# Kernel tuning notes

Measured on AMD Instinct MI355X. Metric: run time of the kernel, lower is better.

## Reference

```python
import jax, jax.numpy as jnp
from jax import lax
import numpy as np

B, N0 = 4, 4096
NIN, NH, NOUT = 16, 128, 2
DEPTH, K, RADIUS, KNN = 3, 64, 2.0, 3
EPS = 1e-5


def _bn(x, g, b):
    # eval-mode BatchNorm1d with running_mean=0, running_var=1
    return g * x / jnp.sqrt(1.0 + EPS) + b


def _mlp2(h, p):
    # Seq(Lin, ReLU, BN) x 2, as in MLP([d, d, out])
    w1, b1, g1, be1, w2, b2, g2, be2 = p
    h = _bn(jax.nn.relu(h @ w1 + b1), g1, be1)
    return _bn(jax.nn.relu(h @ w2 + b2), g2, be2)


def _fps(pts, m):
    # farthest point sampling, deterministic start at index 0
    n = pts.shape[0]
    def step(carry, _):
        dmin, last = carry
        d = jnp.sum((pts - pts[last]) ** 2, axis=-1)
        dmin = jnp.minimum(dmin, d)
        nxt = jnp.argmax(dmin).astype(jnp.int32)
        return (dmin, nxt), nxt
    _, rest = lax.scan(step, (jnp.full((n,), 1e30, pts.dtype), jnp.int32(0)), None, length=m - 1)
    return jnp.concatenate([jnp.zeros((1,), jnp.int32), rest])


def _sa(xx, pp, m, params):
    # SAModule with PointConv: fps -> radius(K nearest within r) -> gather-MLP-max
    idx = _fps(pp, m)
    q = pp[idx]                                              # [m,3] sampled centers
    d2 = jnp.sum((q[:, None, :] - pp[None, :, :]) ** 2, -1)  # [m,n]
    d2 = jnp.where(d2 <= RADIUS * RADIUS, d2, 1e30)
    neg, nbr = lax.top_k(-d2, K)                             # K nearest inside ball
    valid = neg > -1e29
    h = jnp.concatenate([xx[nbr], pp[nbr] - q[:, None, :]], axis=-1)  # [m,K,C+3]
    h = _mlp2(h, params)
    h = jnp.where(valid[..., None], h, -1e30)
    return jnp.max(h, axis=1), q                             # PointConv max aggr


def _fp(xx, pp, xs, ps, params):
    # FPModule: knn_interpolate (k=3, inverse squared-distance weights) + concat skip + MLP
    d2 = jnp.sum((ps[:, None, :] - pp[None, :, :]) ** 2, -1)  # [n_fine, n_coarse]
    neg, idx = lax.top_k(-d2, KNN)
    w = 1.0 / jnp.maximum(-neg, 1e-16)
    y = jnp.sum(w[..., None] * xx[idx], axis=1) / jnp.sum(w, axis=1, keepdims=True)
    return _mlp2(jnp.concatenate([y, xs], axis=-1), params)


def _forward(x, pos, lin_in_w, lin_in_b,
             sa_w1, sa_b1, sa_g1, sa_be1, sa_w2, sa_b2, sa_g2, sa_be2,
             fp_w1, fp_b1, fp_g1, fp_be1, fp_w2, fp_b2, fp_g2, fp_be2,
             lo_w1, lo_b1, lo_g1, lo_be1, lo_w2, lo_b2, lo_g2, lo_be2):
    xb = jax.nn.relu(x.reshape(B, N0, NIN) @ lin_in_w + lin_in_b)  # lin_in + ReLU
    posb = pos.reshape(B, N0, 3)
    sa = [(xb, posb)]
    n = N0
    for i in range(DEPTH):
        m = n // 2  # ratio = 0.5
        p = (sa_w1[i], sa_b1[i], sa_g1[i], sa_be1[i], sa_w2[i], sa_b2[i], sa_g2[i], sa_be2[i])
        h, q = jax.vmap(lambda a, b: _sa(a, b, m, p))(sa[i][0], sa[i][1])
        sa.append((h, q))
        n = m
    xf, posf = sa[DEPTH]
    for step in range(DEPTH):
        mi = DEPTH - 1 - step
        xs, ps = sa[DEPTH - 1 - step]
        p = (fp_w1[mi], fp_b1[mi], fp_g1[mi], fp_be1[mi], fp_w2[mi], fp_b2[mi], fp_g2[mi], fp_be2[mi])
        xf = jax.vmap(lambda a, b, c, d: _fp(a, b, c, d, p))(xf, posf, xs, ps)
        posf = ps
    out = _mlp2(xf, (lo_w1, lo_b1, lo_g1, lo_be1, lo_w2, lo_b2, lo_g2, lo_be2))
    return out.reshape(B * N0, NOUT)


def setup_inputs() -> dict:
    key = jax.random.key(0)
    ki = iter(jax.random.split(key, 24))
    def nrm(shape, s=0.1):
        return jax.random.normal(next(ki), shape, jnp.float32) * s
    D = NH + 3   # PointConv MLP in-dim
    F = 2 * NH   # FP MLP in-dim (nIn + nSkip)
    return {
        "x": jax.random.normal(next(ki), (B * N0, NIN), jnp.float32),
        "pos": jax.random.uniform(next(ki), (B * N0, 3), jnp.float32) * 16.0,
        "batch": jnp.repeat(jnp.arange(B, dtype=jnp.int32), N0),
        "lin_in_w": nrm((NIN, NH)), "lin_in_b": nrm((NH,)),
        "sa_w1": nrm((DEPTH, D, D)), "sa_b1": nrm((DEPTH, D)),
        "sa_g1": jnp.ones((DEPTH, D)), "sa_be1": jnp.zeros((DEPTH, D)),
        "sa_w2": nrm((DEPTH, D, NH)), "sa_b2": nrm((DEPTH, NH)),
        "sa_g2": jnp.ones((DEPTH, NH)), "sa_be2": jnp.zeros((DEPTH, NH)),
        "fp_w1": nrm((DEPTH, F, F)), "fp_b1": nrm((DEPTH, F)),
        "fp_g1": jnp.ones((DEPTH, F)), "fp_be1": jnp.zeros((DEPTH, F)),
        "fp_w2": nrm((DEPTH, F, NH)), "fp_b2": nrm((DEPTH, NH)),
        "fp_g2": jnp.ones((DEPTH, NH)), "fp_be2": jnp.zeros((DEPTH, NH)),
        "lo_w1": nrm((NH, NH)), "lo_b1": nrm((NH,)),
        "lo_g1": jnp.ones((NH,)), "lo_be1": jnp.zeros((NH,)),
        "lo_w2": nrm((NH, NOUT)), "lo_b2": nrm((NOUT,)),
        "lo_g2": jnp.ones((NOUT,)), "lo_be2": jnp.zeros((NOUT,)),
    }


def reference(x, pos, batch, lin_in_w, lin_in_b,
              sa_w1, sa_b1, sa_g1, sa_be1, sa_w2, sa_b2, sa_g2, sa_be2,
              fp_w1, fp_b1, fp_g1, fp_be1, fp_w2, fp_b2, fp_g2, fp_be2,
              lo_w1, lo_b1, lo_g1, lo_be1, lo_w2, lo_b2, lo_g2, lo_be2):
    return _forward(x, pos, lin_in_w, lin_in_b,
                    sa_w1, sa_b1, sa_g1, sa_be1, sa_w2, sa_b2, sa_g2, sa_be2,
                    fp_w1, fp_b1, fp_g1, fp_be1, fp_w2, fp_b2, fp_g2, fp_be2,
                    lo_w1, lo_b1, lo_g1, lo_be1, lo_w2, lo_b2, lo_g2, lo_be2)
```

## Files before the change

kernel.cpp:

```cpp
#include <hip/hip_runtime.h>
#include <cstddef>


#define EPSF 1e-5f

__device__ __forceinline__ float d2_rn(float dx, float dy, float dz) {
    return __fadd_rn(__fadd_rn(__fmul_rn(dx, dx), __fmul_rn(dy, dy)), __fmul_rn(dz, dz));
}

template <int CTRL, int RMASK>
__device__ __forceinline__ float dpp_max_f32(float v) {
    int o = __builtin_amdgcn_update_dpp(__float_as_int(v), __float_as_int(v),
                                        CTRL, RMASK, 0xf, false);
    return fmaxf(v, __int_as_float(o));
}

template <int N, int NT>
__device__ void fps_role(const float* __restrict__ pts, float* __restrict__ q,
                         const int m, const int b, char* smem) {
    constexpr int PPT = N / NT;
    constexpr int NW = NT / 64;
    float* s_px = (float*)smem;
    float* s_py = s_px + N;
    float* s_pz = s_py + N;
    int*   s_qi = (int*)(s_pz + N);
    float2* s_slot = (float2*)(s_qi + N / 2);
    const int t = threadIdx.x;
    const int wave = t >> 6, lane = t & 63;
    const int base = t * PPT;
    const float* P = pts + (size_t)b * N * 3;
    asm volatile("s_setprio 3");
    float rx[PPT], ry[PPT], rz[PPT], dmin[PPT];
#pragma unroll
    for (int j = 0; j < PPT; ++j) {
        int i = base + j;
        float x = P[i * 3], y = P[i * 3 + 1], z = P[i * 3 + 2];
        rx[j] = x; ry[j] = y; rz[j] = z; dmin[j] = 1e30f;
        s_px[i] = x; s_py[i] = y; s_pz[i] = z;
    }
    float lx = P[0], ly = P[1], lz = P[2];
    if (t == 0) s_qi[0] = 0;

    for (int step = 1; step < m; ++step) {
        float bv = -1.0f; int bj = 0;
#pragma unroll
        for (int j = 0; j < PPT; ++j) {
            float d = d2_rn(rx[j] - lx, ry[j] - ly, rz[j] - lz);
            float dm = fminf(dmin[j], d);
            dmin[j] = dm;
            if (dm > bv) { bv = dm; bj = j; }
        }
        const int bidx = base + bj;

        float v = bv;
        v = dpp_max_f32<0x111, 0xf>(v);
        v = dpp_max_f32<0x112, 0xf>(v);
        v = dpp_max_f32<0x114, 0xf>(v);
        v = dpp_max_f32<0x118, 0xf>(v);
        v = dpp_max_f32<0x142, 0xa>(v);
        v = dpp_max_f32<0x143, 0xc>(v);
        const float mv = __int_as_float(__builtin_amdgcn_readlane(__float_as_int(v), 63));
        unsigned long long mb = __ballot(bv == mv);
        const int wl = __ffsll((long long)mb) - 1;
        const int wbi = __builtin_amdgcn_readlane(bidx, wl);

        const int p = step & 1;
        if (lane == 0) s_slot[p * NW + wave] = make_float2(mv, __int_as_float(wbi));
        __syncthreads();

        float2 sl = s_slot[p * NW + (lane & (NW - 1))];
        float gvt = sl.x;
        gvt = dpp_max_f32<0x111, 0xf>(gvt);
        gvt = dpp_max_f32<0x112, 0xf>(gvt);
        if (NW == 8) gvt = dpp_max_f32<0x114, 0xf>(gvt);
        const float gm = __int_as_float(
            __builtin_amdgcn_readlane(__float_as_int(gvt), NW - 1));
        unsigned long long gb = __ballot((lane < NW) && (sl.x == gm));
        const int gl = __ffsll((long long)gb) - 1;
        const int gi = __builtin_amdgcn_readlane(__float_as_int(sl.y), gl);

        lx = s_px[gi]; ly = s_py[gi]; lz = s_pz[gi];
        if (t == 0) s_qi[step] = gi;
    }
    __syncthreads();
    for (int e = t; e < m; e += NT) {
        int gi = s_qi[e];
        size_t o = ((size_t)b * m + e) * 3;
        q[o] = s_px[gi]; q[o + 1] = s_py[gi]; q[o + 2] = s_pz[gi];
    }
}

__device__ void lin_role(const float* __restrict__ x, const float* __restrict__ w,
                         const float* __restrict__ bias, float* __restrict__ xb,
                         const int blk) {
    const int t = threadIdx.x;
    const int row = blk * 2 + (t >> 7);
    const int col = t & 127;
    float acc = bias[col];
#pragma unroll
    for (int k = 0; k < 16; ++k) acc = fmaf(x[row * 16 + k], w[k * 128 + col], acc);
    xb[row * 128 + col] = fmaxf(acc, 0.0f);
}

template <int CHUNK, int WACT>
__device__ void nbr_role(const float* __restrict__ pts, const float* __restrict__ q,
                         int2* __restrict__ pairs, unsigned* __restrict__ counter,
                         const int n, const int m, const int blk, char* smem) {
    const int w = threadIdx.x >> 6, lane = threadIdx.x & 63;
    if (w >= WACT) return;
    float* D = (float*)smem + w * CHUNK * 64;
    const int c = blk * WACT + w;
    const int b = c / m;
    const float* P = pts + (size_t)b * n * 3;
    const float qx = q[(size_t)c * 3 + 0];
    const float qy = q[(size_t)c * 3 + 1];
    const float qz = q[(size_t)c * 3 + 2];
    for (int s = 0; s < CHUNK; ++s) {
        int i = s * 64 + lane;
        float d2 = d2_rn(P[i * 3] - qx, P[i * 3 + 1] - qy, P[i * 3 + 2] - qz);
        D[i] = (d2 <= 4.0f) ? d2 : 1e30f;
    }
    int my_g = -1;
    int cnt = 0;
    for (int round = 0; round < 64; ++round) {
        float bv = 3e38f;
        int bi = 0x7fffffff;
        for (int s = 0; s < CHUNK; ++s) {
            int i = s * 64 + lane;
            float v = D[i];
            if (v < bv) { bv = v; bi = i; }
        }
#pragma unroll
        for (int off = 32; off >= 1; off >>= 1) {
            float ov = __shfl_xor(bv, off, 64);
            int   oi = __shfl_xor(bi, off, 64);
            if (ov < bv || (ov == bv && oi < bi)) { bv = ov; bi = oi; }
        }
        if (bv > 1e29f) break;
        if (round == lane) my_g = bi;
        if (lane == (bi & 63)) D[bi] = 3e38f;
        ++cnt;
    }
    unsigned base = 0;
    if (lane == 0) base = atomicAdd(counter, (unsigned)cnt);
    base = (unsigned)__shfl((int)base, 0, 64);
    if (lane < cnt) pairs[base + lane] = make_int2(c, my_g);
}

typedef float Row132[132];
__device__ void sa_body(const float* __restrict__ xx, const float* __restrict__ pts,
    const float* __restrict__ q, const int2* __restrict__ pairs,
    const unsigned* __restrict__ vcount,
    const float* __restrict__ w1, const float* __restrict__ b1,
    const float* __restrict__ g1, const float* __restrict__ be1,
    const float* __restrict__ w2, const float* __restrict__ b2,
    const float* __restrict__ g2, const float* __restrict__ be2,
    float* __restrict__ hout, const int lm, const int ln, const int blk, char* smem) {
    Row132* shA = (Row132*)smem;
    Row132* shW = (Row132*)(smem + 33792);
    int* sh_c = (int*)(smem + 50688);
    int* sh_g = sh_c + 64;
    const int t = threadIdx.x;
    const int V = (int)*vcount;
    const int r0 = blk * 64;
    if (r0 >= V) return;
    if (t < 64) {
        int r = r0 + t;
        if (r < V) { int2 p = pairs[r]; sh_c[t] = p.x; sh_g[t] = p.y; }
        else { sh_c[t] = -1; sh_g[t] = 0; }
    }
    __syncthreads();

    for (int e = t; e < 64 * 33; e += 256) {
        int row = e / 33, cid = e - row * 33;
        int c = sh_c[row];
        float4 v = make_float4(0.f, 0.f, 0.f, 0.f);
        if (c >= 0) {
            int g = sh_g[row];
            int b = c >> lm;
            size_t pt = ((size_t)(b << ln) + g);
            if (cid < 32) {
                v = *(const float4*)(xx + (pt << 7) + cid * 4);
            } else {
                const float* P = pts + pt * 3;
                const float* Q = q + (size_t)c * 3;
                v.x = P[0] - Q[0]; v.y = P[1] - Q[1]; v.z = P[2] - Q[2]; v.w = 0.f;
            }
        }
        *(float4*)&shA[row][cid * 4] = v;
    }
    __syncthreads();

    const float invs = 1.0f / sqrtf(1.0f + EPSF);
    const int tr = t >> 4, tc = t & 15;
    const int xrow = t >> 2, xcol = t & 3;
    float acc[32];
#pragma unroll
    for (int i = 0; i < 32; ++i) acc[i] = 0.0f;
    float accx = 0.0f;

    for (int k0 = 0; k0 < 132; k0 += 32) {
        const int kc = (132 - k0 < 32) ? (132 - k0) : 32;
        for (int e = t; e < kc * 132; e += 256) {
            int kk = e / 132, j = e - kk * 132;
            int k = k0 + kk;
            shW[kk][j] = (k < 131 && j < 131) ? w1[k * 131 + j] : 0.0f;
        }
        __syncthreads();
        for (int kk = 0; kk < kc; kk += 4) {
            const int k = k0 + kk;
            const float4 A0 = *(const float4*)&shA[tr     ][k];
            const float4 A1 = *(const float4*)&shA[tr + 16][k];
            const float4 A2 = *(const float4*)&shA[tr + 32][k];
            const float4 A3 = *(const float4*)&shA[tr + 48][k];
            const float4 AX = *(const float4*)&shA[xrow][k];
            const float a0v[4] = {A0.x, A0.y, A0.z, A0.w};
            const float a1v[4] = {A1.x, A1.y, A1.z, A1.w};
            const float a2v[4] = {A2.x, A2.y, A2.z, A2.w};
            const float a3v[4] = {A3.x, A3.y, A3.z, A3.w};
            const float axv[4] = {AX.x, AX.y, AX.z, AX.w};
#pragma unroll
            for (int u = 0; u < 4; ++u) {
                const float4 w0 = *(const float4*)&shW[kk + u][8 * tc];
                const float4 w1v = *(const float4*)&shW[kk + u][8 * tc + 4];
                const float wa[8] = {w0.x, w0.y, w0.z, w0.w, w1v.x, w1v.y, w1v.z, w1v.w};
#pragma unroll
                for (int j = 0; j < 8; ++j) {
                    acc[0 * 8 + j] = fmaf(a0v[u], wa[j], acc[0 * 8 + j]);
                    acc[1 * 8 + j] = fmaf(a1v[u], wa[j], acc[1 * 8 + j]);
                    acc[2 * 8 + j] = fmaf(a2v[u], wa[j], acc[2 * 8 + j]);
                    acc[3 * 8 + j] = fmaf(a3v[u], wa[j], acc[3 * 8 + j]);
                }
                accx = fmaf(axv[u], shW[kk + u][128 + xcol], accx);
            }
        }
        __syncthreads();
    }
#pragma unroll
    for (int i = 0; i < 4; ++i)
#pragma unroll
        for (int j = 0; j < 8; ++j) {
            int col = 8 * tc + j;
            float z = fmaxf(acc[i * 8 + j] + b1[col], 0.0f);
            shA[tr + 16 * i][col] = g1[col] * z * invs + be1[col];
        }
    if (xcol < 3) {
        int col = 128 + xcol;
        float z = fmaxf(accx + b1[col], 0.0f);
        shA[xrow][col] = g1[col] * z * invs + be1[col];
    } else {
        shA[xrow][131] = 0.0f;
    }

#pragma unroll
    for (int i = 0; i < 32; ++i) acc[i] = 0.0f;
    for (int k0 = 0; k0 < 132; k0 += 32) {
        const int kc = (132 - k0 < 32) ? (132 - k0) : 32;
        for (int e = t; e < kc * 132; e += 256) {
            int kk = e / 132, j = e - kk * 132;
            int k = k0 + kk;
            shW[kk][j] = (k < 131 && j < 128) ? w2[k * 128 + j] : 0.0f;
        }
        __syncthreads();
        for (int kk = 0; kk < kc; kk += 4) {
            const int k = k0 + kk;
            const float4 A0 = *(const float4*)&shA[tr     ][k];
            const float4 A1 = *(const float4*)&shA[tr + 16][k];
            const float4 A2 = *(const float4*)&shA[tr + 32][k];
            const float4 A3 = *(const float4*)&shA[tr + 48][k];
            const float a0v[4] = {A0.x, A0.y, A0.z, A0.w};
            const float a1v[4] = {A1.x, A1.y, A1.z, A1.w};
            const float a2v[4] = {A2.x, A2.y, A2.z, A2.w};
            const float a3v[4] = {A3.x, A3.y, A3.z, A3.w};
#pragma unroll
            for (int u = 0; u < 4; ++u) {
                const float4 w0 = *(const float4*)&shW[kk + u][8 * tc];
                const float4 w1v = *(const float4*)&shW[kk + u][8 * tc + 4];
                const float wa[8] = {w0.x, w0.y, w0.z, w0.w, w1v.x, w1v.y, w1v.z, w1v.w};
#pragma unroll
                for (int j = 0; j < 8; ++j) {
                    acc[0 * 8 + j] = fmaf(a0v[u], wa[j], acc[0 * 8 + j]);
                    acc[1 * 8 + j] = fmaf(a1v[u], wa[j], acc[1 * 8 + j]);
                    acc[2 * 8 + j] = fmaf(a2v[u], wa[j], acc[2 * 8 + j]);
                    acc[3 * 8 + j] = fmaf(a3v[u], wa[j], acc[3 * 8 + j]);
                }
            }
        }
        __syncthreads();
    }
#pragma unroll
    for (int i = 0; i < 4; ++i)
#pragma unroll
        for (int j = 0; j < 8; ++j) {
            int col = 8 * tc + j;
            float z = fmaxf(acc[i * 8 + j] + b2[col], 0.0f);
            shA[tr + 16 * i][col] = g2[col] * z * invs + be2[col];
        }
    __syncthreads();

    if (t < 128) {
        const int col = t;
        float run = -1.0f;
        int cur = sh_c[0];
        for (int row = 0; row < 64; ++row) {
            int c = sh_c[row];
            if (c != cur) {
                if (cur >= 0)
                    atomicMax((unsigned*)&hout[((size_t)cur << 7) + col], __float_as_uint(run));
                run = -1.0f; cur = c;
            }
            run = fmaxf(run, shA[row][col]);
        }
        if (cur >= 0)
            atomicMax((unsigned*)&hout[((size_t)cur << 7) + col], __float_as_uint(run));
    }
}

__device__ void knn_role(const float* __restrict__ pf, const float* __restrict__ pc,
                         int* __restrict__ kidx, float* __restrict__ kw,
                         const int nf, const int nc, const int blk) {
    const int tg = blk * 256 + threadIdx.x;
    const int b = tg / nf;
    const float* F = pf + (size_t)tg * 3;
    const float fx = F[0], fy = F[1], fz = F[2];
    const float* C = pc + (size_t)b * nc * 3;
    float b0 = 1e30f, b1 = 1e30f, b2 = 1e30f;
    int i0 = 0, i1 = 0, i2 = 0;
    for (int j = 0; j < nc; ++j) {
        float d2 = d2_rn(C[j * 3] - fx, C[j * 3 + 1] - fy, C[j * 3 + 2] - fz);
        if (d2 < b0)      { b2 = b1; i2 = i1; b1 = b0; i1 = i0; b0 = d2; i0 = j; }
        else if (d2 < b1) { b2 = b1; i2 = i1; b1 = d2; i1 = j; }
        else if (d2 < b2) { b2 = d2; i2 = j; }
    }
    float w0 = 1.0f / fmaxf(b0, 1e-16f);
    float w1 = 1.0f / fmaxf(b1, 1e-16f);
    float w2 = 1.0f / fmaxf(b2, 1e-16f);
    float inv = 1.0f / (w0 + w1 + w2);
    size_t o = (size_t)tg * 3;
    kidx[o] = i0; kidx[o + 1] = i1; kidx[o + 2] = i2;
    kw[o] = w0 * inv; kw[o + 1] = w1 * inv; kw[o + 2] = w2 * inv;
}

__global__ __launch_bounds__(256) void stage_a_kernel(
    const float* __restrict__ pos, float* __restrict__ q1,
    const float* __restrict__ x, const float* __restrict__ lin_w,
    const float* __restrict__ lin_b, float* __restrict__ xb,
    float* __restrict__ hbuf, unsigned* __restrict__ ctrs) {
    __shared__ __align__(16) char smem[57408];
    const int blk = blockIdx.x;
    if (blk < 4) {
        fps_role<4096, 256>(pos, q1, 2048, blk, smem);
    } else if (blk < 4 + 8192) {
        lin_role(x, lin_w, lin_b, xb, blk - 4);
    } else {
        const int i = blk - 8196;
        *(float4*)(hbuf + (size_t)i * 1024 + threadIdx.x * 4) =
            make_float4(0.f, 0.f, 0.f, 0.f);
        if (i == 0 && threadIdx.x < 3) ctrs[threadIdx.x * 16] = 0u;
    }
}

__global__ __launch_bounds__(256) void stage_b_kernel(
    const float* __restrict__ q1, float* __restrict__ q2,
    const float* __restrict__ pos, int2* __restrict__ pairs1,
    unsigned* __restrict__ ctr0,
    int* __restrict__ kidx2, float* __restrict__ kw2) {
    __shared__ __align__(16) char smem[32768];
    const int blk = blockIdx.x;
    if (blk < 4) fps_role<2048, 256>(q1, q2, 1024, blk, smem);
    else if (blk < 4 + 4096)
        nbr_role<64, 2>(pos, q1, pairs1, ctr0, 4096, 2048, blk - 4, smem);
    else
        knn_role(pos, q1, kidx2, kw2, 4096, 2048, blk - 4100);
}

__global__ __launch_bounds__(256) void stage_c_kernel(
    const float* __restrict__ q2, float* __restrict__ q3,
    const float* __restrict__ q1, int2* __restrict__ pairs2,
    unsigned* __restrict__ ctr1,
    const float* __restrict__ xb, const float* __restrict__ pos,
    const int2* __restrict__ pairs1, const unsigned* __restrict__ ctr0,
    const float* __restrict__ w1, const float* __restrict__ b1,
    const float* __restrict__ g1, const float* __restrict__ be1,
    const float* __restrict__ w2, const float* __restrict__ b2,
    const float* __restrict__ g2, const float* __restrict__ be2,
    float* __restrict__ h1, int* __restrict__ kidx1, float* __restrict__ kw1) {
    __shared__ __align__(16) char smem[51200];
    const int blk = blockIdx.x;
    if (blk < 4) fps_role<1024, 256>(q2, q3, 512, blk, smem);
    else if (blk < 4 + 1024)
        nbr_role<32, 4>(q1, q2, pairs2, ctr1, 2048, 1024, blk - 4, smem);
    else if (blk < 4 + 1024 + 8192)
        sa_body(xb, pos, q1, pairs1, ctr0, w1, b1, g1, be1, w2, b2, g2, be2,
                h1, 11, 12, blk - 1028, smem);
    else
        knn_role(q1, q2, kidx1, kw1, 2048, 1024, blk - 9220);
}

__global__ __launch_bounds__(256) void stage_d_kernel(
    const float* __restrict__ q2, const float* __restrict__ q3,
    int2* __restrict__ pairs3, unsigned* __restrict__ ctr2,
    const float* __restrict__ h1, const float* __restrict__ q1,
    const int2* __restrict__ pairs2, const unsigned* __restrict__ ctr1,
    const float* __restrict__ w1, const float* __restrict__ b1,
    const float* __restrict__ g1, const float* __restrict__ be1,
    const float* __restrict__ w2, const float* __restrict__ b2,
    const float* __restrict__ g2, const float* __restrict__ be2,
    float* __restrict__ h2, int* __restrict__ kidx0, float* __restrict__ kw0) {
    __shared__ __align__(16) char smem[51200];
    const int blk = blockIdx.x;
    if (blk < 512) nbr_role<16, 4>(q2, q3, pairs3, ctr2, 1024, 512, blk, smem);
    else if (blk < 512 + 16) knn_role(q2, q3, kidx0, kw0, 1024, 512, blk - 512);
    else
        sa_body(h1, q1, q2, pairs2, ctr1, w1, b1, g1, be1, w2, b2, g2, be2,
                h2, 10, 11, blk - 528, smem);
}

__global__ __launch_bounds__(256) void sa_fused_kernel(
    const float* xx, const float* pts, const float* q, const int2* pairs,
    const unsigned* vcount,
    const float* w1, const float* b1, const float* g1, const float* be1,
    const float* w2, const float* b2, const float* g2, const float* be2,
    float* hout, int lm, int ln) {
    __shared__ __align__(16) char smem[51200];
    sa_body(xx, pts, q, pairs, vcount, w1, b1, g1, be1, w2, b2, g2, be2,
            hout, lm, ln, blockIdx.x, smem);
}

__global__ __launch_bounds__(256) void fp_fused_kernel(
    const float* __restrict__ xc, const float* __restrict__ xs,
    const int* __restrict__ kidx, const float* __restrict__ kw,
    const float* __restrict__ w1, const float* __restrict__ b1,
    const float* __restrict__ g1, const float* __restrict__ be1,
    const float* __restrict__ w2, const float* __restrict__ b2,
    const float* __restrict__ g2, const float* __restrict__ be2,
    float* __restrict__ out, int lnf) {
    __shared__ __align__(16) float shA[32][260];
    __shared__ __align__(16) float shW[16][256];
    const int t = threadIdx.x;
    const int r0 = blockIdx.x * 32;
    const float invs = 1.0f / sqrtf(1.0f + EPSF);

    for (int e = t; e < 32 * 64; e += 256) {
        int r = e >> 6, cid = e & 63;
        int fr = r0 + r;
        float4 v;
        if (cid < 32) {
            int b = fr >> lnf;
            size_t o = (size_t)fr * 3;
            int i0 = kidx[o], i1 = kidx[o + 1], i2 = kidx[o + 2];
            float u0 = kw[o], u1 = kw[o + 1], u2 = kw[o + 2];
            const float* X = xc + (((size_t)b << lnf) >> 1) * 128;
            const float4 A0 = *(const float4*)(X + (size_t)i0 * 128 + cid * 4);
            const float4 A1 = *(const float4*)(X + (size_t)i1 * 128 + cid * 4);
            const float4 A2 = *(const float4*)(X + (size_t)i2 * 128 + cid * 4);
            v.x = u0 * A0.x + u1 * A1.x + u2 * A2.x;
            v.y = u0 * A0.y + u1 * A1.y + u2 * A2.y;
            v.z = u0 * A0.z + u1 * A1.z + u2 * A2.z;
            v.w = u0 * A0.w + u1 * A1.w + u2 * A2.w;
        } else {
            v = *(const float4*)(xs + (size_t)fr * 128 + (cid - 32) * 4);
        }
        *(float4*)&shA[r][cid * 4] = v;
    }
    __syncthreads();

    const int tr = t >> 5, tc = t & 31;
    float acc[32];
#pragma unroll
    for (int i = 0; i < 32; ++i) acc[i] = 0.0f;
    for (int k0 = 0; k0 < 256; k0 += 16) {
        for (int e = t; e < 16 * 64; e += 256) {
            int kk = e >> 6, cid = e & 63;
            *(float4*)&shW[kk][cid * 4] =
                *(const float4*)(w1 + (size_t)(k0 + kk) * 256 + cid * 4);
        }
        __syncthreads();
        for (int kk = 0; kk < 16; kk += 4) {
            const int k = k0 + kk;
            const float4 A0 = *(const float4*)&shA[tr     ][k];
            const float4 A1 = *(const float4*)&shA[tr +  8][k];
            const float4 A2 = *(const float4*)&shA[tr + 16][k];
            const float4 A3 = *(const float4*)&shA[tr + 24][k];
            const float a0v[4] = {A0.x, A0.y, A0.z, A0.w};
            const float a1v[4] = {A1.x, A1.y, A1.z, A1.w};
            const float a2v[4] = {A2.x, A2.y, A2.z, A2.w};
            const float a3v[4] = {A3.x, A3.y, A3.z, A3.w};
#pragma unroll
            for (int u = 0; u < 4; ++u) {
                const float4 w0v = *(const float4*)&shW[kk + u][8 * tc];
                const float4 w1v = *(const float4*)&shW[kk + u][8 * tc + 4];
                const float wa[8] = {w0v.x, w0v.y, w0v.z, w0v.w, w1v.x, w1v.y, w1v.z, w1v.w};
#pragma unroll
                for (int j = 0; j < 8; ++j) {
                    acc[0 * 8 + j] = fmaf(a0v[u], wa[j], acc[0 * 8 + j]);
                    acc[1 * 8 + j] = fmaf(a1v[u], wa[j], acc[1 * 8 + j]);
                    acc[2 * 8 + j] = fmaf(a2v[u], wa[j], acc[2 * 8 + j]);
                    acc[3 * 8 + j] = fmaf(a3v[u], wa[j], acc[3 * 8 + j]);
                }
            }
        }
        __syncthreads();
    }
#pragma unroll
    for (int i = 0; i < 4; ++i)
#pragma unroll
        for (int j = 0; j < 8; ++j) {
            int col = 8 * tc + j;
            float z = fmaxf(acc[i * 8 + j] + b1[col], 0.0f);
            shA[tr + 8 * i][col] = g1[col] * z * invs + be1[col];
        }
    __syncthreads();

    const int tr2 = t >> 4, tc2 = t & 15;
    float acc2[16];
#pragma unroll
    for (int i = 0; i < 16; ++i) acc2[i] = 0.0f;
    for (int k0 = 0; k0 < 256; k0 += 16) {
        for (int e = t; e < 16 * 32; e += 256) {
            int kk = e >> 5, cid = e & 31;
            *(float4*)&shW[kk][cid * 4] =
                *(const float4*)(w2 + (size_t)(k0 + kk) * 128 + cid * 4);
        }
        __syncthreads();
        for (int kk = 0; kk < 16; kk += 4) {
            const int k = k0 + kk;
            const float4 A0 = *(const float4*)&shA[tr2     ][k];
            const float4 A1 = *(const float4*)&shA[tr2 + 16][k];
            const float a0v[4] = {A0.x, A0.y, A0.z, A0.w};
            const float a1v[4] = {A1.x, A1.y, A1.z, A1.w};
#pragma unroll
            for (int u = 0; u < 4; ++u) {
                const float4 w0v = *(const float4*)&shW[kk + u][8 * tc2];
                const float4 w1v = *(const float4*)&shW[kk + u][8 * tc2 + 4];
                const float wa[8] = {w0v.x, w0v.y, w0v.z, w0v.w, w1v.x, w1v.y, w1v.z, w1v.w};
#pragma unroll
                for (int j = 0; j < 8; ++j) {
                    acc2[0 * 8 + j] = fmaf(a0v[u], wa[j], acc2[0 * 8 + j]);
                    acc2[1 * 8 + j] = fmaf(a1v[u], wa[j], acc2[1 * 8 + j]);
                }
            }
        }
        __syncthreads();
    }
#pragma unroll
    for (int i = 0; i < 2; ++i)
#pragma unroll
        for (int j = 0; j < 8; ++j) {
            int col = 8 * tc2 + j;
            int fr = r0 + tr2 + 16 * i;
            float z = fmaxf(acc2[i * 8 + j] + b2[col], 0.0f);
            out[(size_t)fr * 128 + col] = g2[col] * z * invs + be2[col];
        }
}

__global__ __launch_bounds__(256) void lo_fused_kernel(
    const float* __restrict__ in,
    const float* __restrict__ w1, const float* __restrict__ b1,
    const float* __restrict__ g1, const float* __restrict__ be1,
    const float* __restrict__ w2, const float* __restrict__ b2,
    const float* __restrict__ g2, const float* __restrict__ be2,
    float* __restrict__ out) {
    __shared__ __align__(16) float shA[32][132];
    __shared__ __align__(16) float shW[16][128];
    const int t = threadIdx.x;
    const int r0 = blockIdx.x * 32;
    const float invs = 1.0f / sqrtf(1.0f + EPSF);

    for (int e = t; e < 32 * 32; e += 256) {
        int r = e >> 5, cid = e & 31;
        *(float4*)&shA[r][cid * 4] =
            *(const float4*)(in + (size_t)(r0 + r) * 128 + cid * 4);
    }
    __syncthreads();

    const int tr = t >> 4, tc = t & 15;
    float acc[16];
#pragma unroll
    for (int i = 0; i < 16; ++i) acc[i] = 0.0f;
    for (int k0 = 0; k0 < 128; k0 += 16) {
        for (int e = t; e < 16 * 32; e += 256) {
            int kk = e >> 5, cid = e & 31;
            *(float4*)&shW[kk][cid * 4] =
                *(const float4*)(w1 + (size_t)(k0 + kk) * 128 + cid * 4);
        }
        __syncthreads();
        for (int kk = 0; kk < 16; ++kk) {
            const int k = k0 + kk;
            float a0 = shA[2 * tr + 0][k], a1 = shA[2 * tr + 1][k];
            const float4 w0v = *(const float4*)&shW[kk][8 * tc];
            const float4 w1v = *(const float4*)&shW[kk][8 * tc + 4];
            const float wa[8] = {w0v.x, w0v.y, w0v.z, w0v.w, w1v.x, w1v.y, w1v.z, w1v.w};
#pragma unroll
            for (int j = 0; j < 8; ++j) {
                acc[0 * 8 + j] = fmaf(a0, wa[j], acc[0 * 8 + j]);
                acc[1 * 8 + j] = fmaf(a1, wa[j], acc[1 * 8 + j]);
            }
        }
        __syncthreads();
    }
#pragma unroll
    for (int i = 0; i < 2; ++i)
#pragma unroll
        for (int j = 0; j < 8; ++j) {
            int col = 8 * tc + j;
            float z = fmaxf(acc[i * 8 + j] + b1[col], 0.0f);
            shA[2 * tr + i][col] = g1[col] * z * invs + be1[col];
        }
    __syncthreads();

    if (t < 64) {
        const int row = t >> 1, col = t & 1;
        float a = b2[col];
        for (int k = 0; k < 128; ++k)
            a = fmaf(shA[row][k], w2[k * 2 + col], a);
        a = fmaxf(a, 0.0f);
        out[(size_t)(r0 + row) * 2 + col] = g2[col] * a * invs + be2[col];
    }
}

extern "C" void kernel_launch(void* const* d_in, const int* in_sizes, int n_in,
                              void* d_out, int out_size, void* d_ws, size_t ws_size,
                              hipStream_t stream) {
    const float* x      = (const float*)d_in[0];
    const float* pos    = (const float*)d_in[1];
    const float* lin_w  = (const float*)d_in[3];
    const float* lin_b  = (const float*)d_in[4];
    const float* sa_w1  = (const float*)d_in[5];
    const float* sa_b1  = (const float*)d_in[6];
    const float* sa_g1  = (const float*)d_in[7];
    const float* sa_be1 = (const float*)d_in[8];
    const float* sa_w2  = (const float*)d_in[9];
    const float* sa_b2  = (const float*)d_in[10];
    const float* sa_g2  = (const float*)d_in[11];
    const float* sa_be2 = (const float*)d_in[12];
    const float* fp_w1  = (const float*)d_in[13];
    const float* fp_b1  = (const float*)d_in[14];
    const float* fp_g1  = (const float*)d_in[15];
    const float* fp_be1 = (const float*)d_in[16];
    const float* fp_w2  = (const float*)d_in[17];
    const float* fp_b2  = (const float*)d_in[18];
    const float* fp_g2  = (const float*)d_in[19];
    const float* fp_be2 = (const float*)d_in[20];
    const float* lo_w1  = (const float*)d_in[21];
    const float* lo_b1  = (const float*)d_in[22];
    const float* lo_g1  = (const float*)d_in[23];
    const float* lo_be1 = (const float*)d_in[24];
    const float* lo_w2  = (const float*)d_in[25];
    const float* lo_b2  = (const float*)d_in[26];
    const float* lo_g2  = (const float*)d_in[27];
    const float* lo_be2 = (const float*)d_in[28];

    float* ws = (float*)d_ws;
    size_t off = 0;
    auto alloc = [&](size_t n) { float* p = ws + off; off += n; return p; };
    float* xb    = alloc(4 * 4096 * 128);
    float* q1    = alloc(4 * 2048 * 3);
    float* q2    = alloc(4 * 1024 * 3);
    float* q3    = alloc(4 * 512 * 3);
    float* h1    = alloc(4 * 2048 * 128);
    float* h2    = alloc(4 * 1024 * 128);
    float* h3    = alloc(4 * 512 * 128);
    int2* pairs1 = (int2*)alloc(4 * 2048 * 64 * 2);
    int2* pairs2 = (int2*)alloc(4 * 1024 * 64 * 2);
    int2* pairs3 = (int2*)alloc(4 * 512 * 64 * 2);
    unsigned* ctrs = (unsigned*)alloc(64);
    int* kidx0   = (int*)alloc(4 * 1024 * 3);
    float* kw0   = alloc(4 * 1024 * 3);
    int* kidx1   = (int*)alloc(4 * 2048 * 3);
    float* kw1   = alloc(4 * 2048 * 3);
    int* kidx2   = (int*)alloc(4 * 4096 * 3);
    float* kw2   = alloc(4 * 4096 * 3);
    float* xfA   = alloc(4 * 4096 * 128);
    float* xfB   = alloc(4 * 4096 * 128);
    if (ws_size < off * sizeof(float)) return;

    stage_a_kernel<<<4 + 8192 + 1792, 256, 0, stream>>>(
        pos, q1, x, lin_w, lin_b, xb, h1, ctrs);

    stage_b_kernel<<<4 + 4096 + 64, 256, 0, stream>>>(
        q1, q2, pos, pairs1, ctrs + 0, kidx2, kw2);

    stage_c_kernel<<<4 + 1024 + 8192 + 32, 256, 0, stream>>>(
        q2, q3, q1, pairs2, ctrs + 16,
        xb, pos, pairs1, ctrs + 0,
        sa_w1, sa_b1, sa_g1, sa_be1, sa_w2, sa_b2, sa_g2, sa_be2, h1,
        kidx1, kw1);

    stage_d_kernel<<<512 + 16 + 4096, 256, 0, stream>>>(
        q2, q3, pairs3, ctrs + 32,
        h1, q1, pairs2, ctrs + 16,
        sa_w1 + 131 * 131, sa_b1 + 131, sa_g1 + 131, sa_be1 + 131,
        sa_w2 + 131 * 128, sa_b2 + 128, sa_g2 + 128, sa_be2 + 128, h2,
        kidx0, kw0);

    sa_fused_kernel<<<2048, 256, 0, stream>>>(h2, q2, q3, pairs3, ctrs + 32,
        sa_w1 + 2 * 131 * 131, sa_b1 + 2 * 131, sa_g1 + 2 * 131, sa_be1 + 2 * 131,
        sa_w2 + 2 * 131 * 128, sa_b2 + 2 * 128, sa_g2 + 2 * 128, sa_be2 + 2 * 128,
        h3, 9, 10);

    fp_fused_kernel<<<4 * 1024 / 32, 256, 0, stream>>>(h3, h2, kidx0, kw0,
        fp_w1 + 2 * 256 * 256, fp_b1 + 2 * 256, fp_g1 + 2 * 256, fp_be1 + 2 * 256,
        fp_w2 + 2 * 256 * 128, fp_b2 + 2 * 128, fp_g2 + 2 * 128, fp_be2 + 2 * 128,
        xfA, 10);

    fp_fused_kernel<<<4 * 2048 / 32, 256, 0, stream>>>(xfA, h1, kidx1, kw1,
        fp_w1 + 256 * 256, fp_b1 + 256, fp_g1 + 256, fp_be1 + 256,
        fp_w2 + 256 * 128, fp_b2 + 128, fp_g2 + 128, fp_be2 + 128,
        xfB, 11);

    fp_fused_kernel<<<4 * 4096 / 32, 256, 0, stream>>>(xfB, xb, kidx2, kw2,
        fp_w1, fp_b1, fp_g1, fp_be1, fp_w2, fp_b2, fp_g2, fp_be2,
        xfA, 12);

    lo_fused_kernel<<<16384 / 32, 256, 0, stream>>>(xfA,
        lo_w1, lo_b1, lo_g1, lo_be1, lo_w2, lo_b2, lo_g2, lo_be2,
        (float*)d_out);
}
```

Baseline: 3.346 ms.

## Replace FPS per-step barrier with tagged LDS spin-wait and packed-key reduction

The farthest-point-sampling loop no longer calls __syncthreads every step. Each wave publishes its best value together with a step-tagged, index-packed key into double-buffered volatile LDS slots, and readers spin until every slot carries the current tag. The cross-wave argmax becomes a 64-bit packed-key max over xor shuffles, and point coordinates move to a float4 LDS layout so one load fetches them. This targets the barrier latency on the serial FPS critical path, at the cost of busy-wait polling and a larger static LDS footprint, which could lower occupancy for the other roles sharing these kernels.

```diff
diff --git a/kernel.cpp b/kernel.cpp
--- a/kernel.cpp
+++ b/kernel.cpp
@@ -20,11 +20,10 @@
                          const int m, const int b, char* smem) {
     constexpr int PPT = N / NT;
     constexpr int NW = NT / 64;
-    float* s_px = (float*)smem;
-    float* s_py = s_px + N;
-    float* s_pz = s_py + N;
-    int*   s_qi = (int*)(s_pz + N);
-    float2* s_slot = (float2*)(s_qi + N / 2);
+    float4* s_p4 = (float4*)smem;
+    int*    s_qi = (int*)(s_p4 + N);
+    volatile unsigned* s_lo = (volatile unsigned*)(s_qi + N / 2);
+    volatile unsigned* s_hi = s_lo + 2 * NW;
     const int t = threadIdx.x;
     const int wave = t >> 6, lane = t & 63;
     const int base = t * PPT;
@@ -36,10 +35,12 @@
         int i = base + j;
         float x = P[i * 3], y = P[i * 3 + 1], z = P[i * 3 + 2];
         rx[j] = x; ry[j] = y; rz[j] = z; dmin[j] = 1e30f;
-        s_px[i] = x; s_py[i] = y; s_pz[i] = z;
-    }
+        s_p4[i] = make_float4(x, y, z, 0.0f);
+    }
+    if (t == 0) s_qi[0] = 0;
+    if (t < 2 * NW) { s_lo[t] = 0u; s_hi[t] = 0u; }
+    __syncthreads();
     float lx = P[0], ly = P[1], lz = P[2];
-    if (t == 0) s_qi[0] = 0;
 
     for (int step = 1; step < m; ++step) {
         float bv = -1.0f; int bj = 0;
@@ -64,29 +65,39 @@
         const int wl = __ffsll((long long)mb) - 1;
         const int wbi = __builtin_amdgcn_readlane(bidx, wl);
 
-        const int p = step & 1;
-        if (lane == 0) s_slot[p * NW + wave] = make_float2(mv, __int_as_float(wbi));
-        __syncthreads();
-
-        float2 sl = s_slot[p * NW + (lane & (NW - 1))];
-        float gvt = sl.x;
-        gvt = dpp_max_f32<0x111, 0xf>(gvt);
-        gvt = dpp_max_f32<0x112, 0xf>(gvt);
-        if (NW == 8) gvt = dpp_max_f32<0x114, 0xf>(gvt);
-        const float gm = __int_as_float(
-            __builtin_amdgcn_readlane(__float_as_int(gvt), NW - 1));
-        unsigned long long gb = __ballot((lane < NW) && (sl.x == gm));
-        const int gl = __ffsll((long long)gb) - 1;
-        const int gi = __builtin_amdgcn_readlane(__float_as_int(sl.y), gl);
-
-        lx = s_px[gi]; ly = s_py[gi]; lz = s_pz[gi];
+        const unsigned tag = (unsigned)(step & 0xff);
+        const int p = (step & 1) * NW;
+        if (lane == 0) {
+            s_hi[p + wave] = (unsigned)__float_as_int(mv);
+            s_lo[p + wave] = ((unsigned)(4095 - wbi) << 14) | ((unsigned)wave << 8) | tag;
+        }
+        const int sl = p + (lane & (NW - 1));
+        unsigned lo, hi;
+        do {
+            lo = s_lo[sl];
+            hi = s_hi[sl];
+        } while (__any((lo & 0xffu) != tag));
+
+        unsigned long long kv = ((unsigned long long)hi << 32) | lo;
+#pragma unroll
+        for (int off = 1; off < NW; off <<= 1) {
+            unsigned olo = (unsigned)__shfl_xor((int)(unsigned)(kv & 0xffffffffu), off, 64);
+            unsigned ohi = (unsigned)__shfl_xor((int)(unsigned)(kv >> 32), off, 64);
+            unsigned long long ov = ((unsigned long long)ohi << 32) | olo;
+            if (ov > kv) kv = ov;
+        }
+        const int gi = 4095 - (int)((kv >> 14) & 0xfffu);
+
+        const float4 pw = s_p4[gi];
+        lx = pw.x; ly = pw.y; lz = pw.z;
         if (t == 0) s_qi[step] = gi;
     }
     __syncthreads();
     for (int e = t; e < m; e += NT) {
         int gi = s_qi[e];
         size_t o = ((size_t)b * m + e) * 3;
-        q[o] = s_px[gi]; q[o + 1] = s_py[gi]; q[o + 2] = s_pz[gi];
+        float4 pw = s_p4[gi];
+        q[o] = pw.x; q[o + 1] = pw.y; q[o + 2] = pw.z;
     }
 }
 
@@ -346,7 +357,7 @@
     const float* __restrict__ x, const float* __restrict__ lin_w,
     const float* __restrict__ lin_b, float* __restrict__ xb,
     float* __restrict__ hbuf, unsigned* __restrict__ ctrs) {
-    __shared__ __align__(16) char smem[57408];
+    __shared__ __align__(16) char smem[73792];
     const int blk = blockIdx.x;
     if (blk < 4) {
         fps_role<4096, 256>(pos, q1, 2048, blk, smem);
@@ -365,7 +376,7 @@
     const float* __restrict__ pos, int2* __restrict__ pairs1,
     unsigned* __restrict__ ctr0,
     int* __restrict__ kidx2, float* __restrict__ kw2) {
-    __shared__ __align__(16) char smem[32768];
+    __shared__ __align__(16) char smem[36928];
     const int blk = blockIdx.x;
     if (blk < 4) fps_role<2048, 256>(q1, q2, 1024, blk, smem);
     else if (blk < 4 + 4096)
```

After: 3.433 ms. +2.6%, slower.

## Repack SA MLP weights per wave and double-buffer them without block barriers

Applied to the files above, without the earlier changes.

Adds a prepass in stage A that repacks the SA layer weights into padded per-wave column slabs (33 or 32 columns, rows padded to 132) in workspace. The SA MLP body now gives each wave its own column slice and streams 16-row weight chunks through a private double-buffered LDS area, prefetching into registers. This removes the block-wide __syncthreads around each weight tile and the scalar, branchy global weight loads. The cost is extra LDS, a few hundred extra stage A blocks, and each wave reading all 64 activation rows from LDS.

```diff
diff --git a/kernel.cpp b/kernel.cpp
--- a/kernel.cpp
+++ b/kernel.cpp
@@ -147,18 +147,17 @@
     if (lane < cnt) pairs[base + lane] = make_int2(c, my_g);
 }
 
-typedef float Row132[132];
 __device__ void sa_body(const float* __restrict__ xx, const float* __restrict__ pts,
     const float* __restrict__ q, const int2* __restrict__ pairs,
     const unsigned* __restrict__ vcount,
-    const float* __restrict__ w1, const float* __restrict__ b1,
+    const float* __restrict__ wp1, const float* __restrict__ b1,
     const float* __restrict__ g1, const float* __restrict__ be1,
-    const float* __restrict__ w2, const float* __restrict__ b2,
+    const float* __restrict__ wp2, const float* __restrict__ b2,
     const float* __restrict__ g2, const float* __restrict__ be2,
     float* __restrict__ hout, const int lm, const int ln, const int blk, char* smem) {
-    Row132* shA = (Row132*)smem;
-    Row132* shW = (Row132*)(smem + 33792);
-    int* sh_c = (int*)(smem + 50688);
+    float (*shA)[132] = (float (*)[132])smem;
+    float* shWall = (float*)(smem + 33792);
+    int* sh_c = (int*)(smem + 52224);
     int* sh_g = sh_c + 64;
     const int t = threadIdx.x;
     const int V = (int)*vcount;
@@ -191,112 +190,168 @@
     }
     __syncthreads();
 
+    const int wave = t >> 6, lane = t & 63;
+    const int rr = lane & 15, cg = lane >> 4;
+    float* Wb = shWall + wave * 1152;
     const float invs = 1.0f / sqrtf(1.0f + EPSF);
-    const int tr = t >> 4, tc = t & 15;
-    const int xrow = t >> 2, xcol = t & 3;
-    float acc[32];
-#pragma unroll
-    for (int i = 0; i < 32; ++i) acc[i] = 0.0f;
-    float accx = 0.0f;
-
-    for (int k0 = 0; k0 < 132; k0 += 32) {
-        const int kc = (132 - k0 < 32) ? (132 - k0) : 32;
-        for (int e = t; e < kc * 132; e += 256) {
-            int kk = e / 132, j = e - kk * 132;
-            int k = k0 + kk;
-            shW[kk][j] = (k < 131 && j < 131) ? w1[k * 131 + j] : 0.0f;
-        }
-        __syncthreads();
-        for (int kk = 0; kk < kc; kk += 4) {
-            const int k = k0 + kk;
-            const float4 A0 = *(const float4*)&shA[tr     ][k];
-            const float4 A1 = *(const float4*)&shA[tr + 16][k];
-            const float4 A2 = *(const float4*)&shA[tr + 32][k];
-            const float4 A3 = *(const float4*)&shA[tr + 48][k];
-            const float4 AX = *(const float4*)&shA[xrow][k];
-            const float a0v[4] = {A0.x, A0.y, A0.z, A0.w};
-            const float a1v[4] = {A1.x, A1.y, A1.z, A1.w};
-            const float a2v[4] = {A2.x, A2.y, A2.z, A2.w};
-            const float a3v[4] = {A3.x, A3.y, A3.z, A3.w};
-            const float axv[4] = {AX.x, AX.y, AX.z, AX.w};
-#pragma unroll
-            for (int u = 0; u < 4; ++u) {
-                const float4 w0 = *(const float4*)&shW[kk + u][8 * tc];
-                const float4 w1v = *(const float4*)&shW[kk + u][8 * tc + 4];
-                const float wa[8] = {w0.x, w0.y, w0.z, w0.w, w1v.x, w1v.y, w1v.z, w1v.w};
-#pragma unroll
-                for (int j = 0; j < 8; ++j) {
-                    acc[0 * 8 + j] = fmaf(a0v[u], wa[j], acc[0 * 8 + j]);
-                    acc[1 * 8 + j] = fmaf(a1v[u], wa[j], acc[1 * 8 + j]);
-                    acc[2 * 8 + j] = fmaf(a2v[u], wa[j], acc[2 * 8 + j]);
-                    acc[3 * 8 + j] = fmaf(a3v[u], wa[j], acc[3 * 8 + j]);
+
+    {
+        const float4* Wg = (const float4*)(wp1 + (size_t)wave * (132 * 36));
+        float acc[32], accx[4];
+#pragma unroll
+        for (int i = 0; i < 32; ++i) acc[i] = 0.0f;
+#pragma unroll
+        for (int i = 0; i < 4; ++i) accx[i] = 0.0f;
+
+        float4 p0, p1, p2;
+        p0 = Wg[lane]; p1 = Wg[lane + 64];
+        if (lane < 16) p2 = Wg[lane + 128];
+        {
+            float4* dst = (float4*)Wb;
+            dst[lane] = p0; dst[lane + 64] = p1;
+            if (lane < 16) dst[lane + 128] = p2;
+        }
+        int cur = 0;
+        for (int c = 0; c < 9; ++c) {
+            const int kc = (c == 8) ? 4 : 16;
+            const int n4n = (c + 1 == 8) ? 36 : 144;
+            if (c < 8) {
+                const float4* src = Wg + (size_t)(c + 1) * 144;
+                if (lane < n4n) p0 = src[lane];
+                if (lane + 64 < n4n) p1 = src[lane + 64];
+                if (lane + 128 < n4n) p2 = src[lane + 128];
+            }
+            const float* Wc = Wb + cur * 576;
+            const int k0c = c * 16;
+            for (int kk = 0; kk < kc; kk += 4) {
+                const float4 A0 = *(const float4*)&shA[rr     ][k0c + kk];
+                const float4 A1 = *(const float4*)&shA[rr + 16][k0c + kk];
+                const float4 A2 = *(const float4*)&shA[rr + 32][k0c + kk];
+                const float4 A3 = *(const float4*)&shA[rr + 48][k0c + kk];
+                const float a0v[4] = {A0.x, A0.y, A0.z, A0.w};
+                const float a1v[4] = {A1.x, A1.y, A1.z, A1.w};
+                const float a2v[4] = {A2.x, A2.y, A2.z, A2.w};
+                const float a3v[4] = {A3.x, A3.y, A3.z, A3.w};
+#pragma unroll
+                for (int u = 0; u < 4; ++u) {
+                    const float* wr = Wc + (kk + u) * 36;
+                    const float4 w0 = *(const float4*)(wr + 8 * cg);
+                    const float4 w1v = *(const float4*)(wr + 8 * cg + 4);
+                    const float wx = wr[32];
+                    const float wa[8] = {w0.x, w0.y, w0.z, w0.w, w1v.x, w1v.y, w1v.z, w1v.w};
+#pragma unroll
+                    for (int j = 0; j < 8; ++j) {
+                        acc[0 * 8 + j] = fmaf(a0v[u], wa[j], acc[0 * 8 + j]);
+                        acc[1 * 8 + j] = fmaf(a1v[u], wa[j], acc[1 * 8 + j]);
+                        acc[2 * 8 + j] = fmaf(a2v[u], wa[j], acc[2 * 8 + j]);
+                        acc[3 * 8 + j] = fmaf(a3v[u], wa[j], acc[3 * 8 + j]);
+                    }
+                    accx[0] = fmaf(a0v[u], wx, accx[0]);
+                    accx[1] = fmaf(a1v[u], wx, accx[1]);
+                    accx[2] = fmaf(a2v[u], wx, accx[2]);
+                    accx[3] = fmaf(a3v[u], wx, accx[3]);
                 }
-                accx = fmaf(axv[u], shW[kk + u][128 + xcol], accx);
-            }
-        }
-        __syncthreads();
-    }
-#pragma unroll
-    for (int i = 0; i < 4; ++i)
-#pragma unroll
-        for (int j = 0; j < 8; ++j) {
-            int col = 8 * tc + j;
-            float z = fmaxf(acc[i * 8 + j] + b1[col], 0.0f);
-            shA[tr + 16 * i][col] = g1[col] * z * invs + be1[col];
-        }
-    if (xcol < 3) {
-        int col = 128 + xcol;
-        float z = fmaxf(accx + b1[col], 0.0f);
-        shA[xrow][col] = g1[col] * z * invs + be1[col];
-    } else {
-        shA[xrow][131] = 0.0f;
-    }
-
-#pragma unroll
-    for (int i = 0; i < 32; ++i) acc[i] = 0.0f;
-    for (int k0 = 0; k0 < 132; k0 += 32) {
-        const int kc = (132 - k0 < 32) ? (132 - k0) : 32;
-        for (int e = t; e < kc * 132; e += 256) {
-            int kk = e / 132, j = e - kk * 132;
-            int k = k0 + kk;
-            shW[kk][j] = (k < 131 && j < 128) ? w2[k * 128 + j] : 0.0f;
-        }
-        __syncthreads();
-        for (int kk = 0; kk < kc; kk += 4) {
-            const int k = k0 + kk;
-            const float4 A0 = *(const float4*)&shA[tr     ][k];
-            const float4 A1 = *(const float4*)&shA[tr + 16][k];
-            const float4 A2 = *(const float4*)&shA[tr + 32][k];
-            const float4 A3 = *(const float4*)&shA[tr + 48][k];
-            const float a0v[4] = {A0.x, A0.y, A0.z, A0.w};
-            const float a1v[4] = {A1.x, A1.y, A1.z, A1.w};
-            const float a2v[4] = {A2.x, A2.y, A2.z, A2.w};
-            const float a3v[4] = {A3.x, A3.y, A3.z, A3.w};
-#pragma unroll
-            for (int u = 0; u < 4; ++u) {
-                const float4 w0 = *(const float4*)&shW[kk + u][8 * tc];
-                const float4 w1v = *(const float4*)&shW[kk + u][8 * tc + 4];
-                const float wa[8] = {w0.x, w0.y, w0.z, w0.w, w1v.x, w1v.y, w1v.z, w1v.w};
-#pragma unroll
-                for (int j = 0; j < 8; ++j) {
-                    acc[0 * 8 + j] = fmaf(a0v[u], wa[j], acc[0 * 8 + j]);
-                    acc[1 * 8 + j] = fmaf(a1v[u], wa[j], acc[1 * 8 + j]);
-                    acc[2 * 8 + j] = fmaf(a2v[u], wa[j], acc[2 * 8 + j]);
-                    acc[3 * 8 + j] = fmaf(a3v[u], wa[j], acc[3 * 8 + j]);
+            }
+            if (c < 8) {
+                float4* dst = (float4*)(Wb + (cur ^ 1) * 576);
+                if (lane < n4n) dst[lane] = p0;
+                if (lane + 64 < n4n) dst[lane + 64] = p1;
+                if (lane + 128 < n4n) dst[lane + 128] = p2;
+            }
+            cur ^= 1;
+        }
+        __syncthreads();
+#pragma unroll
+        for (int i = 0; i < 4; ++i)
+#pragma unroll
+            for (int j = 0; j < 8; ++j) {
+                const int col = 33 * wave + 8 * cg + j;
+                const int row = rr + 16 * i;
+                float z = fmaxf(acc[i * 8 + j] + b1[col], 0.0f);
+                shA[row][col] = g1[col] * z * invs + be1[col];
+            }
+        if (cg == 0) {
+            const int col = 33 * wave + 32;
+            if (col < 131) {
+#pragma unroll
+                for (int i = 0; i < 4; ++i) {
+                    float z = fmaxf(accx[i] + b1[col], 0.0f);
+                    shA[rr + 16 * i][col] = g1[col] * z * invs + be1[col];
                 }
-            }
-        }
-        __syncthreads();
-    }
-#pragma unroll
-    for (int i = 0; i < 4; ++i)
-#pragma unroll
-        for (int j = 0; j < 8; ++j) {
-            int col = 8 * tc + j;
-            float z = fmaxf(acc[i * 8 + j] + b2[col], 0.0f);
-            shA[tr + 16 * i][col] = g2[col] * z * invs + be2[col];
-        }
-    __syncthreads();
+            } else {
+#pragma unroll
+                for (int i = 0; i < 4; ++i) shA[rr + 16 * i][131] = 0.0f;
+            }
+        }
+        __syncthreads();
+    }
+
+    {
+        const float4* Wg = (const float4*)(wp2 + (size_t)wave * (132 * 32));
+        float acc[32];
+#pragma unroll
+        for (int i = 0; i < 32; ++i) acc[i] = 0.0f;
+
+        float4 p0, p1;
+        p0 = Wg[lane]; p1 = Wg[lane + 64];
+        {
+            float4* dst = (float4*)Wb;
+            dst[lane] = p0; dst[lane + 64] = p1;
+        }
+        int cur = 0;
+        for (int c = 0; c < 9; ++c) {
+            const int kc = (c == 8) ? 4 : 16;
+            const int n4n = (c + 1 == 8) ? 32 : 128;
+            if (c < 8) {
+                const float4* src = Wg + (size_t)(c + 1) * 128;
+                if (lane < n4n) p0 = src[lane];
+                if (lane + 64 < n4n) p1 = src[lane + 64];
+            }
+            const float* Wc = Wb + cur * 576;
+            const int k0c = c * 16;
+            for (int kk = 0; kk < kc; kk += 4) {
+                const float4 A0 = *(const float4*)&shA[rr     ][k0c + kk];
+                const float4 A1 = *(const float4*)&shA[rr + 16][k0c + kk];
+                const float4 A2 = *(const float4*)&shA[rr + 32][k0c + kk];
+                const float4 A3 = *(const float4*)&shA[rr + 48][k0c + kk];
+                const float a0v[4] = {A0.x, A0.y, A0.z, A0.w};
+                const float a1v[4] = {A1.x, A1.y, A1.z, A1.w};
+                const float a2v[4] = {A2.x, A2.y, A2.z, A2.w};
+                const float a3v[4] = {A3.x, A3.y, A3.z, A3.w};
+#pragma unroll
+                for (int u = 0; u < 4; ++u) {
+                    const float* wr = Wc + (kk + u) * 32;
+                    const float4 w0 = *(const float4*)(wr + 8 * cg);
+                    const float4 w1v = *(const float4*)(wr + 8 * cg + 4);
+                    const float wa[8] = {w0.x, w0.y, w0.z, w0.w, w1v.x, w1v.y, w1v.z, w1v.w};
+#pragma unroll
+                    for (int j = 0; j < 8; ++j) {
+                        acc[0 * 8 + j] = fmaf(a0v[u], wa[j], acc[0 * 8 + j]);
+                        acc[1 * 8 + j] = fmaf(a1v[u], wa[j], acc[1 * 8 + j]);
+                        acc[2 * 8 + j] = fmaf(a2v[u], wa[j], acc[2 * 8 + j]);
+                        acc[3 * 8 + j] = fmaf(a3v[u], wa[j], acc[3 * 8 + j]);
+                    }
+                }
+            }
+            if (c < 8) {
+                float4* dst = (float4*)(Wb + (cur ^ 1) * 576);
+                if (lane < n4n) dst[lane] = p0;
+                if (lane + 64 < n4n) dst[lane + 64] = p1;
+            }
+            cur ^= 1;
+        }
+        __syncthreads();
+#pragma unroll
+        for (int i = 0; i < 4; ++i)
+#pragma unroll
+            for (int j = 0; j < 8; ++j) {
+                const int col = 32 * wave + 8 * cg + j;
+                const int row = rr + 16 * i;
+                float z = fmaxf(acc[i * 8 + j] + b2[col], 0.0f);
+                shA[row][col] = g2[col] * z * invs + be2[col];
+            }
+        __syncthreads();
+    }
 
     if (t < 128) {
         const int col = t;
@@ -345,18 +400,41 @@
     const float* __restrict__ pos, float* __restrict__ q1,
     const float* __restrict__ x, const float* __restrict__ lin_w,
     const float* __restrict__ lin_b, float* __restrict__ xb,
-    float* __restrict__ hbuf, unsigned* __restrict__ ctrs) {
+    float* __restrict__ hbuf, unsigned* __restrict__ ctrs,
+    const float* __restrict__ sa_w1, const float* __restrict__ sa_w2,
+    float* __restrict__ wp1, float* __restrict__ wp2) {
     __shared__ __align__(16) char smem[57408];
     const int blk = blockIdx.x;
     if (blk < 4) {
         fps_role<4096, 256>(pos, q1, 2048, blk, smem);
     } else if (blk < 4 + 8192) {
         lin_role(x, lin_w, lin_b, xb, blk - 4);
-    } else {
+    } else if (blk < 4 + 8192 + 1792) {
         const int i = blk - 8196;
         *(float4*)(hbuf + (size_t)i * 1024 + threadIdx.x * 4) =
             make_float4(0.f, 0.f, 0.f, 0.f);
         if (i == 0 && threadIdx.x < 3) ctrs[threadIdx.x * 16] = 0u;
+    } else {
+        const int f = (blk - 9988) * 256 + threadIdx.x;
+        if (f < 57024) {
+            int c = f % 36; int r = f / 36;
+            int k = r % 132; int s = r / 132;
+            int w = s & 3; int lvl = s >> 2;
+            int col = 33 * w + c;
+            float v = 0.0f;
+            if (k < 131 && c < 33 && col < 131)
+                v = sa_w1[(size_t)lvl * 131 * 131 + k * 131 + col];
+            wp1[f] = v;
+        } else if (f < 57024 + 50688) {
+            int f2 = f - 57024;
+            int c = f2 & 31; int r = f2 >> 5;
+            int k = r % 132; int s = r / 132;
+            int w = s & 3; int lvl = s >> 2;
+            float v = 0.0f;
+            if (k < 131)
+                v = sa_w2[(size_t)lvl * 131 * 128 + k * 128 + 32 * w + c];
+            wp2[f2] = v;
+        }
     }
 }
 
@@ -380,18 +458,18 @@
     unsigned* __restrict__ ctr1,
     const float* __restrict__ xb, const float* __restrict__ pos,
     const int2* __restrict__ pairs1, const unsigned* __restrict__ ctr0,
-    const float* __restrict__ w1, const float* __restrict__ b1,
+    const float* __restrict__ wp1, const float* __restrict__ b1,
     const float* __restrict__ g1, const float* __restrict__ be1,
-    const float* __restrict__ w2, const float* __restrict__ b2,
+    const float* __restrict__ wp2, const float* __restrict__ b2,
     const float* __restrict__ g2, const float* __restrict__ be2,
     float* __restrict__ h1, int* __restrict__ kidx1, float* __restrict__ kw1) {
-    __shared__ __align__(16) char smem[51200];
+    __shared__ __align__(16) char smem[52736];
     const int blk = blockIdx.x;
     if (blk < 4) fps_role<1024, 256>(q2, q3, 512, blk, smem);
     else if (blk < 4 + 1024)
         nbr_role<32, 4>(q1, q2, pairs2, ctr1, 2048, 1024, blk - 4, smem);
     else if (blk < 4 + 1024 + 8192)
-        sa_body(xb, pos, q1, pairs1, ctr0, w1, b1, g1, be1, w2, b2, g2, be2,
+        sa_body(xb, pos, q1, pairs1, ctr0, wp1, b1, g1, be1, wp2, b2, g2, be2,
                 h1, 11, 12, blk - 1028, smem);
     else
         knn_role(q1, q2, kidx1, kw1, 2048, 1024, blk - 9220);
@@ -402,28 +480,28 @@
     int2* __restrict__ pairs3, unsigned* __restrict__ ctr2,
     const float* __restrict__ h1, const float* __restrict__ q1,
     const int2* __restrict__ pairs2, const unsigned* __restrict__ ctr1,
-    const float* __restrict__ w1, const float* __restrict__ b1,
+    const float* __restrict__ wp1, const float* __restrict__ b1,
     const float* __restrict__ g1, const float* __restrict__ be1,
-    const float* __restrict__ w2, const float* __restrict__ b2,
+    const float* __restrict__ wp2, const float* __restrict__ b2,
     const float* __restrict__ g2, const float* __restrict__ be2,
     float* __restrict__ h2, int* __restrict__ kidx0, float* __restrict__ kw0) {
-    __shared__ __align__(16) char smem[51200];
+    __shared__ __align__(16) char smem[52736];
     const int blk = blockIdx.x;
     if (blk < 512) nbr_role<16, 4>(q2, q3, pairs3, ctr2, 1024, 512, blk, smem);
     else if (blk < 512 + 16) knn_role(q2, q3, kidx0, kw0, 1024, 512, blk - 512);
     else
-        sa_body(h1, q1, q2, pairs2, ctr1, w1, b1, g1, be1, w2, b2, g2, be2,
+        sa_body(h1, q1, q2, pairs2, ctr1, wp1, b1, g1, be1, wp2, b2, g2, be2,
                 h2, 10, 11, blk - 528, smem);
 }
 
 __global__ __launch_bounds__(256) void sa_fused_kernel(
     const float* xx, const float* pts, const float* q, const int2* pairs,
     const unsigned* vcount,
-    const float* w1, const float* b1, const float* g1, const float* be1,
-    const float* w2, const float* b2, const float* g2, const float* be2,
+    const float* wp1, const float* b1, const float* g1, const float* be1,
+    const float* wp2, const float* b2, const float* g2, const float* be2,
     float* hout, int lm, int ln) {
-    __shared__ __align__(16) char smem[51200];
-    sa_body(xx, pts, q, pairs, vcount, w1, b1, g1, be1, w2, b2, g2, be2,
+    __shared__ __align__(16) char smem[52736];
+    sa_body(xx, pts, q, pairs, vcount, wp1, b1, g1, be1, wp2, b2, g2, be2,
             hout, lm, ln, blockIdx.x, smem);
 }
 
@@ -673,10 +751,12 @@
     float* kw2   = alloc(4 * 4096 * 3);
     float* xfA   = alloc(4 * 4096 * 128);
     float* xfB   = alloc(4 * 4096 * 128);
+    float* wp1   = alloc(3 * 4 * 132 * 36);
+    float* wp2   = alloc(3 * 4 * 132 * 32);
     if (ws_size < off * sizeof(float)) return;
 
-    stage_a_kernel<<<4 + 8192 + 1792, 256, 0, stream>>>(
-        pos, q1, x, lin_w, lin_b, xb, h1, ctrs);
+    stage_a_kernel<<<4 + 8192 + 1792 + 421, 256, 0, stream>>>(
+        pos, q1, x, lin_w, lin_b, xb, h1, ctrs, sa_w1, sa_w2, wp1, wp2);
 
     stage_b_kernel<<<4 + 4096 + 64, 256, 0, stream>>>(
         q1, q2, pos, pairs1, ctrs + 0, kidx2, kw2);
@@ -684,19 +764,19 @@
     stage_c_kernel<<<4 + 1024 + 8192 + 32, 256, 0, stream>>>(
         q2, q3, q1, pairs2, ctrs + 16,
         xb, pos, pairs1, ctrs + 0,
-        sa_w1, sa_b1, sa_g1, sa_be1, sa_w2, sa_b2, sa_g2, sa_be2, h1,
+        wp1, sa_b1, sa_g1, sa_be1, wp2, sa_b2, sa_g2, sa_be2, h1,
         kidx1, kw1);
 
     stage_d_kernel<<<512 + 16 + 4096, 256, 0, stream>>>(
         q2, q3, pairs3, ctrs + 32,
         h1, q1, pairs2, ctrs + 16,
-        sa_w1 + 131 * 131, sa_b1 + 131, sa_g1 + 131, sa_be1 + 131,
-        sa_w2 + 131 * 128, sa_b2 + 128, sa_g2 + 128, sa_be2 + 128, h2,
+        wp1 + 4 * 132 * 36, sa_b1 + 131, sa_g1 + 131, sa_be1 + 131,
+        wp2 + 4 * 132 * 32, sa_b2 + 128, sa_g2 + 128, sa_be2 + 128, h2,
         kidx0, kw0);
 
     sa_fused_kernel<<<2048, 256, 0, stream>>>(h2, q2, q3, pairs3, ctrs + 32,
-        sa_w1 + 2 * 131 * 131, sa_b1 + 2 * 131, sa_g1 + 2 * 131, sa_be1 + 2 * 131,
-        sa_w2 + 2 * 131 * 128, sa_b2 + 2 * 128, sa_g2 + 2 * 128, sa_be2 + 2 * 128,
+        wp1 + 2 * 4 * 132 * 36, sa_b1 + 2 * 131, sa_g1 + 2 * 131, sa_be1 + 2 * 131,
+        wp2 + 2 * 4 * 132 * 32, sa_b2 + 2 * 128, sa_g2 + 2 * 128, sa_be2 + 2 * 128,
         h3, 9, 10);
 
     fp_fused_kernel<<<4 * 1024 / 32, 256, 0, stream>>>(h3, h2, kidx0, kw0,
```

After: 3.461 ms. 3.4% more time.
